# Performance work log

Measured on AMD Instinct MI355X. Metric: run time of the kernel, lower is better.

## Reference

```python
import jax, jax.numpy as jnp
import numpy as np

B, D = 512, 512
NOBJ, NWRD = 12, 16  # word_feat rows act as 'objects', object_feat rows as 'words' (arg swap in SentiGAT.forward)
N_OW = NOBJ + NWRD
EPS = 1e-12


def _with_self_loops(src, dst, n):
    return (np.concatenate([src, np.arange(n)]), np.concatenate([dst, np.arange(n)]))

_src = np.tile(np.arange(NOBJ), NWRD)                 # arange(n_obj).repeat(n_words) in torch == tile
_dst = np.repeat(np.arange(NWRD), NOBJ) + NOBJ        # repeat_interleave + offset
SRC_OW, DST_OW = map(jnp.asarray, _with_self_loops(_src, _dst, N_OW))

_E5 = np.array([[0,0,0,0,1,1,1,1,2,2,2,2,3,3,3,3,4,4,4,4],
                [1,2,3,4,0,2,3,4,0,1,3,4,0,1,2,4,0,1,2,3]])
SRC5, DST5 = map(jnp.asarray, _with_self_loops(_E5[0], _E5[1], 5))


def gat_conv(x, src, dst, W, a_src, a_dst, bias, concat, num_nodes):
    """PyG GATConv (add_self_loops already in src/dst, negative_slope=0.2, dropout=0)."""
    heads, out_dim = a_src.shape
    h = (x @ W).reshape(num_nodes, heads, out_dim)
    e = jax.nn.leaky_relu((h * a_src).sum(-1)[src] + (h * a_dst).sum(-1)[dst], 0.2)  # [E, heads]
    m = jax.ops.segment_max(e, dst, num_segments=num_nodes)
    p = jnp.exp(e - m[dst])
    alpha = p / jax.ops.segment_sum(p, dst, num_segments=num_nodes)[dst]             # softmax over incoming edges
    out = jax.ops.segment_sum(alpha[:, :, None] * h[src], dst, num_segments=num_nodes)
    out = out.reshape(num_nodes, heads * out_dim) if concat else out.mean(axis=1)
    return out + bias


def _ind_norm(f):
    # add_feature_indicator + F.normalize(p=2, dim=1, eps=1e-12)
    v = (f.sum(axis=1) != 0).astype(f.dtype)[:, None]
    g = jnp.concatenate([f, v], axis=1)
    return g / jnp.maximum(jnp.linalg.norm(g, axis=1, keepdims=True), EPS)


def setup_inputs() -> dict:
    k = jax.random.split(jax.random.key(0), 32)
    r = lambda i, s: jax.random.normal(k[i], s, dtype=jnp.float32)
    sc = 0.05
    return {
        "text_feat": r(0, (B, D)), "image_feat": r(1, (B, D)), "imgtxt_feat": r(2, (B, D)),
        "face_feat": r(3, (B, D)), "word_feat": r(4, (B, NOBJ, D)), "object_feat": r(5, (B, NWRD, D)),
        "ow_W": r(6, (D, 2 * D)) * sc, "ow_asrc": r(7, (2, D)) * sc, "ow_adst": r(8, (2, D)) * sc,
        "ow_b": jnp.zeros((D,), jnp.float32),
        "g1_W": r(9, (D + 1, D)) * sc, "g1_asrc": r(10, (1, D)) * sc, "g1_adst": r(11, (1, D)) * sc,
        "g1_b": jnp.zeros((D,), jnp.float32),
        "g2_W": r(12, (D, D)) * sc, "g2_asrc": r(13, (1, D)) * sc, "g2_adst": r(14, (1, D)) * sc,
        "g2_b": jnp.zeros((D,), jnp.float32),
        "m1_W": r(15, (5 * D, D)) * sc, "m1_b": jnp.zeros((D,), jnp.float32),
        "m2_W": r(16, (D, 3)) * sc, "m2_b": jnp.zeros((3,), jnp.float32),
    }


def reference(text_feat, image_feat, imgtxt_feat, face_feat, word_feat, object_feat,
              ow_W, ow_asrc, ow_adst, ow_b,
              g1_W, g1_asrc, g1_adst, g1_b,
              g2_W, g2_asrc, g2_adst, g2_b,
              m1_W, m1_b, m2_W, m2_b):
    # --- ObjectWordGAT (object_embs=word_feat, word_embs=object_feat per SentiGAT.forward) ---
    def per_sample(obj, wrd):
        x = jnp.concatenate([obj, wrd], axis=0)                       # [N_OW, D]
        h = gat_conv(x, SRC_OW, DST_OW, ow_W, ow_asrc, ow_adst, ow_b, False, N_OW)
        uo, uw = h[:NOBJ], h[NOBJ:]
        attn = jax.nn.softmax(uo @ uw.T, axis=1)                      # [NOBJ, NWRD]
        return (attn @ uw).mean(axis=0)                               # [D]
    aligned = jax.vmap(per_sample)(word_feat, object_feat)            # [B, D]

    feats = [_ind_norm(f) for f in (text_feat, image_feat, imgtxt_feat, face_feat, aligned)]
    x = jnp.stack(feats, axis=1)                                      # [B, 5, D+1]

    # edge_attr (cosine sims) is ignored by GATConv when edge_dim is None
    def graph5(xb):
        h = gat_conv(xb, SRC5, DST5, g1_W, g1_asrc, g1_adst, g1_b, True, 5)
        h = jax.nn.relu(h)
        return gat_conv(h, SRC5, DST5, g2_W, g2_asrc, g2_adst, g2_b, True, 5)
    x = jax.vmap(graph5)(x)                                           # [B, 5, D]

    fused = x.reshape(B, 5 * D)
    hid = jax.nn.relu(fused @ m1_W + m1_b)                            # dropout = identity (eval)
    return hid @ m2_W + m2_b                                          # [B, 3] logits
```

## Files before the change

kernel.cpp:

```cpp
#include <hip/hip_runtime.h>
#include <hip/hip_bf16.h>
#include <math.h>


#define B_SAMP 512

typedef short short8 __attribute__((ext_vector_type(8)));
typedef float floatx4 __attribute__((ext_vector_type(4)));

__device__ __forceinline__ float lrelu02(float x) { return x > 0.f ? x : 0.2f * x; }

__device__ __forceinline__ unsigned short cvt_bf16(float f) {
    union { float f; unsigned int u; } v; v.f = f;
    unsigned int u = v.u;
    return (unsigned short)((u + 0x7FFFu + ((u >> 16) & 1u)) >> 16);
}
__device__ __forceinline__ float bf2f(unsigned short u) {
    union { unsigned int u; float f; } v; v.u = ((unsigned int)u) << 16;
    return v.f;
}
__device__ __forceinline__ void gload_lds16(const unsigned short* g, unsigned short* l) {
    __builtin_amdgcn_global_load_lds(
        (const __attribute__((address_space(1))) void*)g,
        (__attribute__((address_space(3))) void*)l, 16, 0, 0);
}

__global__ __launch_bounds__(256) void prep(
    const float* __restrict__ ow_W, const float* __restrict__ ow_asrc,
    const float* __restrict__ ow_adst,
    const float* __restrict__ g1_W, const float* __restrict__ g2_W,
    const float* __restrict__ m1_W,
    float* __restrict__ vg, unsigned short* __restrict__ owWt,
    unsigned short* __restrict__ g1Wt, unsigned short* __restrict__ g2Wt,
    unsigned short* __restrict__ m1Wt)
{
    __shared__ float T[32][33];
    const int tid = threadIdx.x;
    int bid = blockIdx.x;

    if (bid < 128) {
        const int lane = tid & 63;
        const int gw = bid * 4 + (tid >> 6);
        for (int idx = gw; idx < 2048; idx += 512) {
            int t = idx >> 9, k = idx & 511;
            const float* a = (t < 2) ? (ow_asrc + t * 512) : (ow_adst + (t - 2) * 512);
            const float* wr = ow_W + (size_t)k * 1024 + (t & 1) * 512;
            float s = 0.f;
#pragma unroll
            for (int j = 0; j < 8; ++j) s += wr[lane + 64 * j] * a[lane + 64 * j];
            for (int off = 32; off > 0; off >>= 1) s += __shfl_down(s, off, 64);
            if (lane == 0) vg[idx] = s;
        }
        return;
    }
    bid -= 128;
    const float* W; int ldw, K, Kpad, koff, ktiles; float scale; unsigned short* Wt;
    if (bid < 256)        { W = ow_W;       ldw = 1024; K = 512;  Kpad = 1024; koff = 0;   scale = 0.5f; Wt = owWt; ktiles = 16; }
    else if (bid < 512)   { bid -= 256;  W = ow_W + 512; ldw = 1024; K = 512;  Kpad = 1024; koff = 512; scale = 0.5f; Wt = owWt; ktiles = 16; }
    else if (bid < 784)   { bid -= 512;  W = g1_W; ldw = 512; K = 513;  Kpad = 544;  koff = 0; scale = 1.f; Wt = g1Wt; ktiles = 17; }
    else if (bid < 1040)  { bid -= 784;  W = g2_W; ldw = 512; K = 512;  Kpad = 512;  koff = 0; scale = 1.f; Wt = g2Wt; ktiles = 16; }
    else                  { bid -= 1040; W = m1_W; ldw = 512; K = 2560; Kpad = 2560; koff = 0; scale = 1.f; Wt = m1Wt; ktiles = 80; }
    const int k0 = (bid % ktiles) * 32;
    const int n0 = (bid / ktiles) * 32;
    {
        int kr = tid >> 3, nc = (tid & 7) * 4;
        float4 v = make_float4(0.f, 0.f, 0.f, 0.f);
        if (k0 + kr < K) v = *(const float4*)(W + (size_t)(k0 + kr) * ldw + n0 + nc);
        T[nc + 0][kr] = v.x * scale; T[nc + 1][kr] = v.y * scale;
        T[nc + 2][kr] = v.z * scale; T[nc + 3][kr] = v.w * scale;
    }
    __syncthreads();
    {
        int nr = tid >> 3, kc = (tid & 7) * 4;
        ushort4 w;
        w.x = cvt_bf16(T[nr][kc + 0]);
        w.y = cvt_bf16(T[nr][kc + 1]);
        w.z = cvt_bf16(T[nr][kc + 2]);
        w.w = cvt_bf16(T[nr][kc + 3]);
        *(ushort4*)(Wt + (size_t)(n0 + nr) * Kpad + koff + k0 + kc) = w;
    }
}

__global__ __launch_bounds__(256) void ow_pre(
    const float* __restrict__ wf, const float* __restrict__ of,
    const float* __restrict__ vg,
    unsigned short* __restrict__ zcat)
{
    const int b = blockIdx.x;
    __shared__ float Xs[28][512];
    __shared__ float ss[28][2], sd[28][2];
    __shared__ float alpha[16][2][13];

    const int tid = threadIdx.x;
    const int lane = tid & 63;
    const int wid = tid >> 6;

    for (int idx = tid; idx < 28 * 128; idx += 256) {
        int n = idx >> 7, c = (idx & 127) * 4;
        const float* src = (n < 12) ? (wf + ((size_t)b * 12 + n) * 512)
                                    : (of + ((size_t)b * 16 + (n - 12)) * 512);
        *(float4*)&Xs[n][c] = *(const float4*)(src + c);
    }
    __syncthreads();

    for (int p = wid; p < 112; p += 4) {
        int n = p >> 2, t = p & 3;
        const float* vv = vg + t * 512;
        float s = 0.f;
#pragma unroll
        for (int j = 0; j < 8; ++j) s += Xs[n][lane + 64 * j] * vv[lane + 64 * j];
        for (int off = 32; off > 0; off >>= 1) s += __shfl_down(s, off, 64);
        if (lane == 0) { if (t < 2) ss[n][t] = s; else sd[n][t - 2] = s; }
    }
    __syncthreads();

    if (tid < 32) {
        int w = tid >> 1, h = tid & 1;
        float sdv = sd[12 + w][h];
        float e[13], mx = -1e30f;
        for (int j = 0; j < 12; ++j) { e[j] = lrelu02(ss[j][h] + sdv); mx = fmaxf(mx, e[j]); }
        e[12] = lrelu02(ss[12 + w][h] + sdv); mx = fmaxf(mx, e[12]);
        float den = 0.f;
        for (int j = 0; j < 13; ++j) { e[j] = expf(e[j] - mx); den += e[j]; }
        float inv = 1.f / den;
        for (int j = 0; j < 13; ++j) alpha[w][h][j] = e[j] * inv;
    }
    __syncthreads();

    unsigned short* zb = zcat + (size_t)b * 28 * 1024;
    for (int idx = tid; idx < 12 * 1024; idx += 256) {
        int n = idx >> 10, d = idx & 511;
        zb[idx] = cvt_bf16(Xs[n][d]);
    }
    for (int c = tid; c < 1024; c += 256) {
        int h = c >> 9, d = c & 511;
        float xr[12];
#pragma unroll
        for (int j = 0; j < 12; ++j) xr[j] = Xs[j][d];
#pragma unroll 4
        for (int w = 0; w < 16; ++w) {
            float a = alpha[w][h][12] * Xs[12 + w][d];
#pragma unroll
            for (int j = 0; j < 12; ++j) a += alpha[w][h][j] * xr[j];
            zb[(size_t)(12 + w) * 1024 + c] = cvt_bf16(a);
        }
    }
}

__global__ __launch_bounds__(256) void gemm_glds(
    const unsigned short* __restrict__ A, int lda,
    const unsigned short* __restrict__ Bt, int ldbt,
    unsigned short* __restrict__ C, int ldc,
    int K, const float* __restrict__ bias)
{
    __shared__ unsigned short As[2][64][32];
    __shared__ unsigned short Bs[2][128][32];

    const int tid = threadIdx.x;
    const int lane = tid & 63;
    const int wid = tid >> 6;

    const int bid = blockIdx.x;
    const int m = (bid >> 5) * 8 + (bid & 7);
    const int n = (bid >> 3) & 3;
    const int m0 = m * 64;
    const int n0 = n * 128;

    const int srow = lane >> 2;
    const int sseg = (lane & 3) * 8;
    const unsigned short* ga = A + (size_t)(m0 + wid * 16 + srow) * lda + sseg;
    const unsigned short* gb = Bt + (size_t)(n0 + wid * 32 + srow) * ldbt + sseg;
    const size_t b16 = (size_t)16 * ldbt;

#define STAGE(t, K0)                                              \
    do {                                                          \
        gload_lds16(ga + (K0), &As[t][wid * 16][0]);              \
        gload_lds16(gb + (K0), &Bs[t][wid * 32][0]);              \
        gload_lds16(gb + (K0) + b16, &Bs[t][wid * 32 + 16][0]);   \
    } while (0)

    const int wm = (wid & 1) * 32;
    const int wn = (wid >> 1) * 64;
    const int fr = lane & 15;
    const int kq = (lane >> 4) * 8;

    floatx4 acc[2][4];
#pragma unroll
    for (int i = 0; i < 2; ++i)
#pragma unroll
        for (int j = 0; j < 4; ++j) acc[i][j] = (floatx4){0.f, 0.f, 0.f, 0.f};

    STAGE(0, 0);
    __syncthreads();

    int t = 0;
    for (int k0 = 0; k0 < K; k0 += 32, t ^= 1) {
        if (k0 + 32 < K) STAGE(t ^ 1, k0 + 32);

        short8 af[2], bw[4];
#pragma unroll
        for (int i = 0; i < 2; ++i)
            af[i] = *(const short8*)&As[t][wm + i * 16 + fr][kq];
#pragma unroll
        for (int j = 0; j < 4; ++j)
            bw[j] = *(const short8*)&Bs[t][wn + j * 16 + fr][kq];
#pragma unroll
        for (int i = 0; i < 2; ++i)
#pragma unroll
            for (int j = 0; j < 4; ++j)
                acc[i][j] = __builtin_amdgcn_mfma_f32_16x16x32_bf16(
                    af[i], bw[j], acc[i][j], 0, 0, 0);
        __syncthreads();
    }
#undef STAGE

    const int fq = lane >> 4;
#pragma unroll
    for (int i = 0; i < 2; ++i) {
#pragma unroll
        for (int j = 0; j < 4; ++j) {
#pragma unroll
            for (int q = 0; q < 4; ++q) {
                int row = m0 + wm + i * 16 + fq * 4 + q;
                int col = n0 + wn + j * 16 + fr;
                C[(size_t)row * ldc + col] = cvt_bf16(acc[i][j][q] + bias[col]);
            }
        }
    }
}

template <int BM, int BN, int WGM, int RELU, int SPLITK, int OBF16>
__global__ __launch_bounds__(256) void gemm_v3(
    const unsigned short* __restrict__ A, int lda,
    const unsigned short* __restrict__ Bt, int ldbt,
    void* __restrict__ Cv, int ldc,
    int M, int N, int K,
    const float* __restrict__ bias)
{
    constexpr int WGN = 4 / WGM;
    constexpr int WM = BM / WGM, WN = BN / WGN;
    constexpr int MF = WM / 16, NF = WN / 16;
    constexpr int CA = (BM * 4 + 255) / 256, CB = (BN * 4 + 255) / 256;

    __shared__ unsigned short As[2][BM][40];
    __shared__ unsigned short Bs[2][BN][40];

    const int tid = threadIdx.x;
    const int m0 = blockIdx.x * BM;
    const int n0 = blockIdx.y * BN;
    const int lane = tid & 63;
    const int wid = tid >> 6;
    const int wm = (wid % WGM) * WM;
    const int wn = (wid / WGM) * WN;
    const int fr = lane & 15;
    const int kq = (lane >> 4) * 8;

    const int kchunk = K / SPLITK;
    const int kbeg = (SPLITK > 1) ? blockIdx.z * kchunk : 0;
    const int kend = kbeg + kchunk;
    float* Cf = (float*)Cv;
    unsigned short* Cb = (unsigned short*)Cv;
    if (SPLITK > 1) Cf += (size_t)blockIdx.z * M * ldc;

    short8 ra[CA], rb[CB];
#define LOADAB(K0)                                                                       \
    do {                                                                                 \
        _Pragma("unroll")                                                                \
        for (int c = 0; c < CA; ++c) {                                                   \
            int id = tid + c * 256;                                                      \
            if (BM * 4 % 256 == 0 || id < BM * 4)                                        \
                ra[c] = *(const short8*)(A + (size_t)(m0 + (id >> 2)) * lda + (K0) + (id & 3) * 8); \
        }                                                                                \
        _Pragma("unroll")                                                                \
        for (int c = 0; c < CB; ++c) {                                                   \
            int id = tid + c * 256;                                                      \
            if (BN * 4 % 256 == 0 || id < BN * 4)                                        \
                rb[c] = *(const short8*)(Bt + (size_t)(n0 + (id >> 2)) * ldbt + (K0) + (id & 3) * 8); \
        }                                                                                \
    } while (0)

    LOADAB(kbeg);

    floatx4 acc[MF][NF];
#pragma unroll
    for (int i = 0; i < MF; ++i)
#pragma unroll
        for (int j = 0; j < NF; ++j) acc[i][j] = (floatx4){0.f, 0.f, 0.f, 0.f};

    int t = 0;
    for (int k0 = kbeg; k0 < kend; k0 += 32, t ^= 1) {
#pragma unroll
        for (int c = 0; c < CA; ++c) {
            int id = tid + c * 256;
            if (BM * 4 % 256 == 0 || id < BM * 4)
                *(short8*)&As[t][id >> 2][(id & 3) * 8] = ra[c];
        }
#pragma unroll
        for (int c = 0; c < CB; ++c) {
            int id = tid + c * 256;
            if (BN * 4 % 256 == 0 || id < BN * 4)
                *(short8*)&Bs[t][id >> 2][(id & 3) * 8] = rb[c];
        }
        __syncthreads();
        if (k0 + 32 < kend) LOADAB(k0 + 32);

        short8 af[MF], bw[NF];
#pragma unroll
        for (int i = 0; i < MF; ++i)
            af[i] = *(const short8*)&As[t][wm + i * 16 + fr][kq];
#pragma unroll
        for (int j = 0; j < NF; ++j)
            bw[j] = *(const short8*)&Bs[t][wn + j * 16 + fr][kq];
#pragma unroll
        for (int i = 0; i < MF; ++i)
#pragma unroll
            for (int j = 0; j < NF; ++j)
                acc[i][j] = __builtin_amdgcn_mfma_f32_16x16x32_bf16(
                    af[i], bw[j], acc[i][j], 0, 0, 0);
    }
#undef LOADAB

    const int fq = lane >> 4;
#pragma unroll
    for (int i = 0; i < MF; ++i) {
#pragma unroll
        for (int j = 0; j < NF; ++j) {
#pragma unroll
            for (int q = 0; q < 4; ++q) {
                int row = m0 + wm + i * 16 + fq * 4 + q;
                int col = n0 + wn + j * 16 + fr;
                float v = acc[i][j][q];
                if (SPLITK == 1 && bias) v += bias[col];
                if (RELU) v = fmaxf(v, 0.f);
                if (OBF16) Cb[(size_t)row * ldc + col] = cvt_bf16(v);
                else       Cf[(size_t)row * ldc + col] = v;
            }
        }
    }
}

__global__ __launch_bounds__(256) void attn_x5(
    const unsigned short* __restrict__ hout,
    const float* __restrict__ tf, const float* __restrict__ im,
    const float* __restrict__ it, const float* __restrict__ fa,
    unsigned short* __restrict__ x5)
{
    const int b = blockIdx.x;
    __shared__ float uo[12][520];
    __shared__ float uw[16][520];
    __shared__ float S[12][16];
    __shared__ float w16[16];
    __shared__ float al[512];

    const int tid = threadIdx.x;
    const int lane = tid & 63;
    const int wid = tid >> 6;
    const unsigned short* hb = hout + (size_t)b * 28 * 512;

    for (int idx = tid; idx < 28 * 64; idx += 256) {
        int n = idx >> 6, c = (idx & 63) * 8;
        short8 v = *(const short8*)(hb + (size_t)n * 512 + c);
        float* row = (n < 12) ? &uo[n][c] : &uw[n - 12][c];
#pragma unroll
        for (int j = 0; j < 8; ++j) row[j] = bf2f((unsigned short)v[j]);
    }
    __syncthreads();

    for (int p = wid; p < 192; p += 4) {
        int i = p >> 4, j = p & 15;
        const float* ua = &uo[i][lane * 8];
        const float* uc = &uw[j][lane * 8];
        float s = 0.f;
#pragma unroll
        for (int d = 0; d < 8; ++d) s += ua[d] * uc[d];
        for (int off = 32; off > 0; off >>= 1) s += __shfl_down(s, off, 64);
        if (lane == 0) S[i][j] = s;
    }
    __syncthreads();

    if (tid < 12) {
        float mx = -1e30f;
        for (int j = 0; j < 16; ++j) mx = fmaxf(mx, S[tid][j]);
        float den = 0.f;
        for (int j = 0; j < 16; ++j) { float p = expf(S[tid][j] - mx); S[tid][j] = p; den += p; }
        float inv = 1.f / den;
        for (int j = 0; j < 16; ++j) S[tid][j] *= inv;
    }
    __syncthreads();

    if (tid < 16) {
        float s = 0.f;
        for (int i = 0; i < 12; ++i) s += S[i][tid];
        w16[tid] = s * (1.f / 12.f);
    }
    __syncthreads();

    for (int d = tid; d < 512; d += 256) {
        float s = 0.f;
#pragma unroll
        for (int j = 0; j < 16; ++j) s += w16[j] * uw[j][d];
        al[d] = s;
    }
    __syncthreads();

    for (int f = wid; f < 5; f += 4) {
        const float* src = (f == 0) ? tf : (f == 1) ? im : (f == 2) ? it : (f == 3) ? fa : nullptr;
        float vals[8];
        float sum = 0.f, sq = 0.f;
#pragma unroll
        for (int j = 0; j < 8; ++j) {
            float v = (f < 4) ? src[(size_t)b * 512 + lane + 64 * j] : al[lane + 64 * j];
            vals[j] = v;
            sum += v;
            sq += v * v;
        }
#pragma unroll
        for (int off = 32; off > 0; off >>= 1) {
            sum += __shfl_xor(sum, off, 64);
            sq  += __shfl_xor(sq,  off, 64);
        }
        float v = (sum != 0.f) ? 1.f : 0.f;
        float nrm = fmaxf(sqrtf(sq + v * v), 1e-12f);
        float inv = 1.f / nrm;
        unsigned short* dst = x5 + ((size_t)b * 5 + f) * 544;
#pragma unroll
        for (int j = 0; j < 8; ++j) dst[lane + 64 * j] = cvt_bf16(vals[j] * inv);
        if (lane == 0) dst[512] = cvt_bf16(v * inv);
        else if (lane < 32) dst[512 + lane] = 0;
    }
}

template <int RELU>
__global__ __launch_bounds__(256) void g5_gat(
    const unsigned short* __restrict__ Hg,
    const float* __restrict__ asrc, const float* __restrict__ adst,
    const float* __restrict__ bias, unsigned short* __restrict__ outp)
{
    const int b = blockIdx.x;
    __shared__ float ss[5], sd[5];
    __shared__ float alpha[5][5];

    const int tid = threadIdx.x;
    const int lane = tid & 63;
    const int wave = tid >> 6;
    const unsigned short* Hb = Hg + (size_t)b * 5 * 512;

    for (int p = wave; p < 10; p += 4) {
        int n = p >> 1, ty = p & 1;
        const unsigned short* hv = Hb + n * 512;
        const float* av = ty ? adst : asrc;
        float s = 0.f;
#pragma unroll
        for (int j = 0; j < 8; ++j) s += bf2f(hv[lane + 64 * j]) * av[lane + 64 * j];
        for (int off = 32; off > 0; off >>= 1) s += __shfl_down(s, off, 64);
        if (lane == 0) { if (ty) sd[n] = s; else ss[n] = s; }
    }
    __syncthreads();

    if (tid < 5) {
        int dn = tid;
        float e[5];
        float mx = -1e30f;
        for (int s = 0; s < 5; ++s) {
            e[s] = lrelu02(ss[s] + sd[dn]);
            mx = fmaxf(mx, e[s]);
        }
        float den = 0.f;
        for (int s = 0; s < 5; ++s) { e[s] = expf(e[s] - mx); den += e[s]; }
        float inv = 1.f / den;
        for (int s = 0; s < 5; ++s) alpha[dn][s] = e[s] * inv;
    }
    __syncthreads();

    for (int d = tid; d < 512; d += 256) {
        float h0 = bf2f(Hb[0 * 512 + d]), h1 = bf2f(Hb[1 * 512 + d]), h2 = bf2f(Hb[2 * 512 + d]);
        float h3 = bf2f(Hb[3 * 512 + d]), h4 = bf2f(Hb[4 * 512 + d]);
        float bd = bias[d];
#pragma unroll
        for (int dn = 0; dn < 5; ++dn) {
            float v = alpha[dn][0] * h0 + alpha[dn][1] * h1 + alpha[dn][2] * h2 +
                      alpha[dn][3] * h3 + alpha[dn][4] * h4 + bd;
            if (RELU) v = fmaxf(v, 0.f);
            outp[((size_t)b * 5 + dn) * 512 + d] = cvt_bf16(v);
        }
    }
}

__global__ __launch_bounds__(64) void final2(
    const float* __restrict__ parts, const float* __restrict__ b1,
    const float* __restrict__ w, const float* __restrict__ bvec,
    float* __restrict__ out)
{
    const int b = blockIdx.x;
    const int lane = threadIdx.x;
    float a0 = 0.f, a1 = 0.f, a2 = 0.f;
#pragma unroll
    for (int j = 0; j < 8; ++j) {
        int d = lane + 64 * j;
        size_t o = (size_t)b * 512 + d;
        float x = parts[o] + parts[262144 + o] + parts[524288 + o] + parts[786432 + o] + b1[d];
        x = fmaxf(x, 0.f);
        a0 += x * w[d * 3 + 0];
        a1 += x * w[d * 3 + 1];
        a2 += x * w[d * 3 + 2];
    }
    for (int off = 32; off > 0; off >>= 1) {
        a0 += __shfl_down(a0, off, 64);
        a1 += __shfl_down(a1, off, 64);
        a2 += __shfl_down(a2, off, 64);
    }
    if (lane == 0) {
        out[b * 3 + 0] = a0 + bvec[0];
        out[b * 3 + 1] = a1 + bvec[1];
        out[b * 3 + 2] = a2 + bvec[2];
    }
}

extern "C" void kernel_launch(void* const* d_in, const int* in_sizes, int n_in,
                              void* d_out, int out_size, void* d_ws, size_t ws_size,
                              hipStream_t stream) {
    const float* text   = (const float*)d_in[0];
    const float* image  = (const float*)d_in[1];
    const float* imgtxt = (const float*)d_in[2];
    const float* face   = (const float*)d_in[3];
    const float* word   = (const float*)d_in[4];
    const float* obj    = (const float*)d_in[5];
    const float* ow_W    = (const float*)d_in[6];
    const float* ow_asrc = (const float*)d_in[7];
    const float* ow_adst = (const float*)d_in[8];
    const float* ow_b    = (const float*)d_in[9];
    const float* g1_W    = (const float*)d_in[10];
    const float* g1_asrc = (const float*)d_in[11];
    const float* g1_adst = (const float*)d_in[12];
    const float* g1_b    = (const float*)d_in[13];
    const float* g2_W    = (const float*)d_in[14];
    const float* g2_asrc = (const float*)d_in[15];
    const float* g2_adst = (const float*)d_in[16];
    const float* g2_b    = (const float*)d_in[17];
    const float* m1_W    = (const float*)d_in[18];
    const float* m1_b    = (const float*)d_in[19];
    const float* m2_W    = (const float*)d_in[20];
    const float* m2_b    = (const float*)d_in[21];

    float* ws = (float*)d_ws;
    float* vg = ws;
    float* hidp = ws + 2048;
    unsigned short* owWt = (unsigned short*)(hidp + 1048576);
    unsigned short* g1Wt = owWt + 524288;
    unsigned short* g2Wt = g1Wt + 278528;
    unsigned short* m1Wt = g2Wt + 262144;
    unsigned short* zcat = m1Wt + 1310720;
    unsigned short* houtb = zcat + 14680064;
    unsigned short* x5b  = houtb + 7340032;
    unsigned short* h1b  = x5b + 1392640;
    unsigned short* fsb  = h1b + 1310720;
    unsigned short* hgb  = fsb + 1310720;

    prep<<<2448, 256, 0, stream>>>(ow_W, ow_asrc, ow_adst, g1_W, g2_W, m1_W,
                                   vg, owWt, g1Wt, g2Wt, m1Wt);

    ow_pre<<<B_SAMP, 256, 0, stream>>>(word, obj, vg, zcat);
    gemm_glds<<<896, 256, 0, stream>>>(
        zcat, 1024, owWt, 1024, houtb, 512, 1024, ow_b);
    attn_x5<<<B_SAMP, 256, 0, stream>>>(houtb, text, image, imgtxt, face, x5b);

    gemm_v3<64, 64, 2, 0, 1, 1><<<dim3(40, 8), 256, 0, stream>>>(
        x5b, 544, g1Wt, 544, hgb, 512, 2560, 512, 544, nullptr);
    g5_gat<1><<<B_SAMP, 256, 0, stream>>>(hgb, g1_asrc, g1_adst, g1_b, h1b);
    gemm_v3<64, 64, 2, 0, 1, 1><<<dim3(40, 8), 256, 0, stream>>>(
        h1b, 512, g2Wt, 512, hgb, 512, 2560, 512, 512, nullptr);
    g5_gat<0><<<B_SAMP, 256, 0, stream>>>(hgb, g2_asrc, g2_adst, g2_b, fsb);

    gemm_v3<64, 64, 2, 0, 4, 0><<<dim3(8, 8, 4), 256, 0, stream>>>(
        fsb, 2560, m1Wt, 2560, hidp, 512, 512, 512, 2560, nullptr);
    final2<<<B_SAMP, 64, 0, stream>>>(hidp, m1_b, m2_W, m2_b, (float*)d_out);
}
```

Before: 128.6 us.

## Exploit self-loop-only object nodes: halve K via pre-summed head weights

Object nodes in the word-object GAT only receive their self-loop, so their head-mean output equals x·(W_h0+W_h1)/2. Prep now builds a pre-summed bf16 weight (WsR) and a second GEMM branch multiplies the raw fp32 word features by it with K=512, instead of carrying them through the concatenated K=1024 path. The zcat buffer shrinks to word rows only, and attn_x5 reads the two separate outputs. This cuts GEMM FLOPs and memory traffic for 12 of the 28 nodes per sample, but the new branch uses register-staged loads with inline fp32-to-bf16 conversion rather than direct global-to-LDS loads.

```diff
diff --git a/kernel.cpp b/kernel.cpp
--- a/kernel.cpp
+++ b/kernel.cpp
@@ -32,15 +32,16 @@
     const float* __restrict__ m1_W,
     float* __restrict__ vg, unsigned short* __restrict__ owWt,
     unsigned short* __restrict__ g1Wt, unsigned short* __restrict__ g2Wt,
-    unsigned short* __restrict__ m1Wt)
+    unsigned short* __restrict__ m1Wt, unsigned short* __restrict__ WsR)
 {
     __shared__ float T[32][33];
     const int tid = threadIdx.x;
     int bid = blockIdx.x;
+    const int lane = tid & 63;
+    const int wid = tid >> 6;
 
     if (bid < 128) {
-        const int lane = tid & 63;
-        const int gw = bid * 4 + (tid >> 6);
+        const int gw = bid * 4 + wid;
         for (int idx = gw; idx < 2048; idx += 512) {
             int t = idx >> 9, k = idx & 511;
             const float* a = (t < 2) ? (ow_asrc + t * 512) : (ow_adst + (t - 2) * 512);
@@ -55,17 +56,25 @@
     }
     bid -= 128;
     const float* W; int ldw, K, Kpad, koff, ktiles; float scale; unsigned short* Wt;
+    int sumh = 0;
     if (bid < 256)        { W = ow_W;       ldw = 1024; K = 512;  Kpad = 1024; koff = 0;   scale = 0.5f; Wt = owWt; ktiles = 16; }
     else if (bid < 512)   { bid -= 256;  W = ow_W + 512; ldw = 1024; K = 512;  Kpad = 1024; koff = 512; scale = 0.5f; Wt = owWt; ktiles = 16; }
     else if (bid < 784)   { bid -= 512;  W = g1_W; ldw = 512; K = 513;  Kpad = 544;  koff = 0; scale = 1.f; Wt = g1Wt; ktiles = 17; }
     else if (bid < 1040)  { bid -= 784;  W = g2_W; ldw = 512; K = 512;  Kpad = 512;  koff = 0; scale = 1.f; Wt = g2Wt; ktiles = 16; }
-    else                  { bid -= 1040; W = m1_W; ldw = 512; K = 2560; Kpad = 2560; koff = 0; scale = 1.f; Wt = m1Wt; ktiles = 80; }
+    else if (bid < 2320)  { bid -= 1040; W = m1_W; ldw = 512; K = 2560; Kpad = 2560; koff = 0; scale = 1.f; Wt = m1Wt; ktiles = 80; }
+    else                  { bid -= 2320; W = ow_W; ldw = 1024; K = 512; Kpad = 512; koff = 0; scale = 0.5f; Wt = WsR; ktiles = 16; sumh = 1; }
     const int k0 = (bid % ktiles) * 32;
     const int n0 = (bid / ktiles) * 32;
     {
         int kr = tid >> 3, nc = (tid & 7) * 4;
         float4 v = make_float4(0.f, 0.f, 0.f, 0.f);
-        if (k0 + kr < K) v = *(const float4*)(W + (size_t)(k0 + kr) * ldw + n0 + nc);
+        if (k0 + kr < K) {
+            v = *(const float4*)(W + (size_t)(k0 + kr) * ldw + n0 + nc);
+            if (sumh) {
+                float4 v2 = *(const float4*)(W + (size_t)(k0 + kr) * ldw + 512 + n0 + nc);
+                v.x += v2.x; v.y += v2.y; v.z += v2.z; v.w += v2.w;
+            }
+        }
         T[nc + 0][kr] = v.x * scale; T[nc + 1][kr] = v.y * scale;
         T[nc + 2][kr] = v.z * scale; T[nc + 3][kr] = v.w * scale;
     }
@@ -81,10 +90,10 @@
     }
 }
 
-__global__ __launch_bounds__(256) void ow_pre(
+__global__ __launch_bounds__(256) void ow_zw(
     const float* __restrict__ wf, const float* __restrict__ of,
     const float* __restrict__ vg,
-    unsigned short* __restrict__ zcat)
+    unsigned short* __restrict__ zw)
 {
     const int b = blockIdx.x;
     __shared__ float Xs[28][512];
@@ -127,31 +136,37 @@
     }
     __syncthreads();
 
-    unsigned short* zb = zcat + (size_t)b * 28 * 1024;
-    for (int idx = tid; idx < 12 * 1024; idx += 256) {
-        int n = idx >> 10, d = idx & 511;
-        zb[idx] = cvt_bf16(Xs[n][d]);
-    }
-    for (int c = tid; c < 1024; c += 256) {
-        int h = c >> 9, d = c & 511;
-        float xr[12];
-#pragma unroll
-        for (int j = 0; j < 12; ++j) xr[j] = Xs[j][d];
+    const int c4 = tid * 4;
+    const int h = tid >> 7;
+    const int d = c4 & 511;
+    float4 xr[12];
+#pragma unroll
+    for (int j = 0; j < 12; ++j) xr[j] = *(const float4*)&Xs[j][d];
+    unsigned short* zb = zw + (size_t)b * 16 * 1024;
 #pragma unroll 4
-        for (int w = 0; w < 16; ++w) {
-            float a = alpha[w][h][12] * Xs[12 + w][d];
-#pragma unroll
-            for (int j = 0; j < 12; ++j) a += alpha[w][h][j] * xr[j];
-            zb[(size_t)(12 + w) * 1024 + c] = cvt_bf16(a);
-        }
-    }
-}
-
-__global__ __launch_bounds__(256) void gemm_glds(
-    const unsigned short* __restrict__ A, int lda,
-    const unsigned short* __restrict__ Bt, int ldbt,
-    unsigned short* __restrict__ C, int ldc,
-    int K, const float* __restrict__ bias)
+    for (int w = 0; w < 16; ++w) {
+        const float* al = &alpha[w][h][0];
+        float4 xw = *(const float4*)&Xs[12 + w][d];
+        float a0 = al[12] * xw.x, a1 = al[12] * xw.y, a2 = al[12] * xw.z, a3 = al[12] * xw.w;
+#pragma unroll
+        for (int j = 0; j < 12; ++j) {
+            a0 += al[j] * xr[j].x; a1 += al[j] * xr[j].y;
+            a2 += al[j] * xr[j].z; a3 += al[j] * xr[j].w;
+        }
+        ushort4 o;
+        o.x = cvt_bf16(a0); o.y = cvt_bf16(a1); o.z = cvt_bf16(a2); o.w = cvt_bf16(a3);
+        *(ushort4*)(zb + (size_t)w * 1024 + c4) = o;
+    }
+}
+
+__global__ __launch_bounds__(256) void gemm_a1(
+    const unsigned short* __restrict__ zw,
+    const unsigned short* __restrict__ owWt,
+    const float* __restrict__ word,
+    const unsigned short* __restrict__ WsR,
+    const float* __restrict__ bias,
+    unsigned short* __restrict__ houtW,
+    unsigned short* __restrict__ houtO)
 {
     __shared__ unsigned short As[2][64][32];
     __shared__ unsigned short Bs[2][128][32];
@@ -159,73 +174,217 @@
     const int tid = threadIdx.x;
     const int lane = tid & 63;
     const int wid = tid >> 6;
-
     const int bid = blockIdx.x;
-    const int m = (bid >> 5) * 8 + (bid & 7);
-    const int n = (bid >> 3) & 3;
-    const int m0 = m * 64;
-    const int n0 = n * 128;
-
-    const int srow = lane >> 2;
-    const int sseg = (lane & 3) * 8;
-    const unsigned short* ga = A + (size_t)(m0 + wid * 16 + srow) * lda + sseg;
-    const unsigned short* gb = Bt + (size_t)(n0 + wid * 32 + srow) * ldbt + sseg;
-    const size_t b16 = (size_t)16 * ldbt;
-
-#define STAGE(t, K0)                                              \
+
+    const int wm = (wid & 1) * 32;
+    const int wn = (wid >> 1) * 64;
+    const int fr = lane & 15;
+    const int kq = (lane >> 4) * 8;
+    const int fq = lane >> 4;
+
+    floatx4 acc[2][4];
+#pragma unroll
+    for (int i = 0; i < 2; ++i)
+#pragma unroll
+        for (int j = 0; j < 4; ++j) acc[i][j] = (floatx4){0.f, 0.f, 0.f, 0.f};
+
+    if (bid < 512) {
+        const int m0 = (bid & 127) * 64;
+        const int n0 = (bid >> 7) * 128;
+        const int srow = lane >> 2;
+        const int sseg = (lane & 3) * 8;
+        const unsigned short* ga = zw + (size_t)(m0 + wid * 16 + srow) * 1024 + sseg;
+        const unsigned short* gb = owWt + (size_t)(n0 + wid * 32 + srow) * 1024 + sseg;
+        const size_t b16 = (size_t)16 * 1024;
+
+#define STAGEW(t, K0)                                             \
     do {                                                          \
         gload_lds16(ga + (K0), &As[t][wid * 16][0]);              \
         gload_lds16(gb + (K0), &Bs[t][wid * 32][0]);              \
         gload_lds16(gb + (K0) + b16, &Bs[t][wid * 32 + 16][0]);   \
     } while (0)
 
-    const int wm = (wid & 1) * 32;
-    const int wn = (wid >> 1) * 64;
-    const int fr = lane & 15;
-    const int kq = (lane >> 4) * 8;
-
-    floatx4 acc[2][4];
-#pragma unroll
-    for (int i = 0; i < 2; ++i)
-#pragma unroll
-        for (int j = 0; j < 4; ++j) acc[i][j] = (floatx4){0.f, 0.f, 0.f, 0.f};
-
-    STAGE(0, 0);
-    __syncthreads();
-
-    int t = 0;
-    for (int k0 = 0; k0 < K; k0 += 32, t ^= 1) {
-        if (k0 + 32 < K) STAGE(t ^ 1, k0 + 32);
-
-        short8 af[2], bw[4];
+        STAGEW(0, 0);
+        __syncthreads();
+        int t = 0;
+        for (int k0 = 0; k0 < 1024; k0 += 32, t ^= 1) {
+            if (k0 + 32 < 1024) STAGEW(t ^ 1, k0 + 32);
+            short8 af[2], bw[4];
+#pragma unroll
+            for (int i = 0; i < 2; ++i)
+                af[i] = *(const short8*)&As[t][wm + i * 16 + fr][kq];
+#pragma unroll
+            for (int j = 0; j < 4; ++j)
+                bw[j] = *(const short8*)&Bs[t][wn + j * 16 + fr][kq];
+#pragma unroll
+            for (int i = 0; i < 2; ++i)
+#pragma unroll
+                for (int j = 0; j < 4; ++j)
+                    acc[i][j] = __builtin_amdgcn_mfma_f32_16x16x32_bf16(
+                        af[i], bw[j], acc[i][j], 0, 0, 0);
+            __syncthreads();
+        }
+#undef STAGEW
 #pragma unroll
         for (int i = 0; i < 2; ++i)
-            af[i] = *(const short8*)&As[t][wm + i * 16 + fr][kq];
-#pragma unroll
-        for (int j = 0; j < 4; ++j)
-            bw[j] = *(const short8*)&Bs[t][wn + j * 16 + fr][kq];
+#pragma unroll
+            for (int j = 0; j < 4; ++j)
+#pragma unroll
+                for (int q = 0; q < 4; ++q) {
+                    int row = m0 + wm + i * 16 + fq * 4 + q;
+                    int col = n0 + wn + j * 16 + fr;
+                    houtW[(size_t)row * 512 + col] = cvt_bf16(acc[i][j][q] + bias[col]);
+                }
+    } else {
+        const int tb = bid - 512;
+        const int m0 = (tb % 96) * 64;
+        const int n0 = (tb / 96) * 128;
+
+        float4 raf[2]; short8 rb[2];
+#define LOADO(K0)                                                                  \
+    do {                                                                           \
+        _Pragma("unroll")                                                          \
+        for (int c = 0; c < 2; ++c) {                                              \
+            int id = tid + c * 256;                                                \
+            raf[c] = *(const float4*)(word + (size_t)(m0 + (id >> 3)) * 512 + (K0) + (id & 7) * 4); \
+            rb[c]  = *(const short8*)(WsR + (size_t)(n0 + (id >> 2)) * 512 + (K0) + (id & 3) * 8);  \
+        }                                                                          \
+    } while (0)
+
+        LOADO(0);
+        int t = 0;
+        for (int k0 = 0; k0 < 512; k0 += 32, t ^= 1) {
+#pragma unroll
+            for (int c = 0; c < 2; ++c) {
+                int id = tid + c * 256;
+                ushort4 w;
+                w.x = cvt_bf16(raf[c].x); w.y = cvt_bf16(raf[c].y);
+                w.z = cvt_bf16(raf[c].z); w.w = cvt_bf16(raf[c].w);
+                *(ushort4*)&As[t][id >> 3][(id & 7) * 4] = w;
+                *(short8*)&Bs[t][id >> 2][(id & 3) * 8] = rb[c];
+            }
+            __syncthreads();
+            if (k0 + 32 < 512) LOADO(k0 + 32);
+            short8 af[2], bw[4];
+#pragma unroll
+            for (int i = 0; i < 2; ++i)
+                af[i] = *(const short8*)&As[t][wm + i * 16 + fr][kq];
+#pragma unroll
+            for (int j = 0; j < 4; ++j)
+                bw[j] = *(const short8*)&Bs[t][wn + j * 16 + fr][kq];
+#pragma unroll
+            for (int i = 0; i < 2; ++i)
+#pragma unroll
+                for (int j = 0; j < 4; ++j)
+                    acc[i][j] = __builtin_amdgcn_mfma_f32_16x16x32_bf16(
+                        af[i], bw[j], acc[i][j], 0, 0, 0);
+        }
+#undef LOADO
 #pragma unroll
         for (int i = 0; i < 2; ++i)
 #pragma unroll
             for (int j = 0; j < 4; ++j)
-                acc[i][j] = __builtin_amdgcn_mfma_f32_16x16x32_bf16(
-                    af[i], bw[j], acc[i][j], 0, 0, 0);
-        __syncthreads();
-    }
-#undef STAGE
-
-    const int fq = lane >> 4;
-#pragma unroll
-    for (int i = 0; i < 2; ++i) {
-#pragma unroll
-        for (int j = 0; j < 4; ++j) {
-#pragma unroll
-            for (int q = 0; q < 4; ++q) {
-                int row = m0 + wm + i * 16 + fq * 4 + q;
-                int col = n0 + wn + j * 16 + fr;
-                C[(size_t)row * ldc + col] = cvt_bf16(acc[i][j][q] + bias[col]);
-            }
-        }
+#pragma unroll
+                for (int q = 0; q < 4; ++q) {
+                    int row = m0 + wm + i * 16 + fq * 4 + q;
+                    int col = n0 + wn + j * 16 + fr;
+                    houtO[(size_t)row * 512 + col] = cvt_bf16(acc[i][j][q] + bias[col]);
+                }
+    }
+}
+
+__global__ __launch_bounds__(256) void attn_x5(
+    const unsigned short* __restrict__ houtO,
+    const unsigned short* __restrict__ houtW,
+    const float* __restrict__ tf, const float* __restrict__ im,
+    const float* __restrict__ it, const float* __restrict__ fa,
+    unsigned short* __restrict__ x5)
+{
+    const int b = blockIdx.x;
+    __shared__ float uo[12][520];
+    __shared__ float uw[16][520];
+    __shared__ float S[12][16];
+    __shared__ float w16[16];
+    __shared__ float al[512];
+
+    const int tid = threadIdx.x;
+    const int lane = tid & 63;
+    const int wid = tid >> 6;
+    const unsigned short* ho = houtO + (size_t)b * 12 * 512;
+    const unsigned short* hw = houtW + (size_t)b * 16 * 512;
+
+    for (int idx = tid; idx < 28 * 64; idx += 256) {
+        int n = idx >> 6, c = (idx & 63) * 8;
+        const unsigned short* src = (n < 12) ? (ho + (size_t)n * 512 + c)
+                                             : (hw + (size_t)(n - 12) * 512 + c);
+        short8 v = *(const short8*)src;
+        float* row = (n < 12) ? &uo[n][c] : &uw[n - 12][c];
+#pragma unroll
+        for (int j = 0; j < 8; ++j) row[j] = bf2f((unsigned short)v[j]);
+    }
+    __syncthreads();
+
+    for (int p = wid; p < 192; p += 4) {
+        int i = p >> 4, j = p & 15;
+        const float* ua = &uo[i][lane * 8];
+        const float* uc = &uw[j][lane * 8];
+        float s = 0.f;
+#pragma unroll
+        for (int d = 0; d < 8; ++d) s += ua[d] * uc[d];
+        for (int off = 32; off > 0; off >>= 1) s += __shfl_down(s, off, 64);
+        if (lane == 0) S[i][j] = s;
+    }
+    __syncthreads();
+
+    if (tid < 12) {
+        float mx = -1e30f;
+        for (int j = 0; j < 16; ++j) mx = fmaxf(mx, S[tid][j]);
+        float den = 0.f;
+        for (int j = 0; j < 16; ++j) { float p = expf(S[tid][j] - mx); S[tid][j] = p; den += p; }
+        float inv = 1.f / den;
+        for (int j = 0; j < 16; ++j) S[tid][j] *= inv;
+    }
+    __syncthreads();
+
+    if (tid < 16) {
+        float s = 0.f;
+        for (int i = 0; i < 12; ++i) s += S[i][tid];
+        w16[tid] = s * (1.f / 12.f);
+    }
+    __syncthreads();
+
+    for (int d = tid; d < 512; d += 256) {
+        float s = 0.f;
+#pragma unroll
+        for (int j = 0; j < 16; ++j) s += w16[j] * uw[j][d];
+        al[d] = s;
+    }
+    __syncthreads();
+
+    for (int f = wid; f < 5; f += 4) {
+        const float* src = (f == 0) ? tf : (f == 1) ? im : (f == 2) ? it : (f == 3) ? fa : nullptr;
+        float vals[8];
+        float sum = 0.f, sq = 0.f;
+#pragma unroll
+        for (int j = 0; j < 8; ++j) {
+            float v = (f < 4) ? src[(size_t)b * 512 + lane + 64 * j] : al[lane + 64 * j];
+            vals[j] = v;
+            sum += v;
+            sq += v * v;
+        }
+#pragma unroll
+        for (int off = 32; off > 0; off >>= 1) {
+            sum += __shfl_xor(sum, off, 64);
+            sq  += __shfl_xor(sq,  off, 64);
+        }
+        float v = (sum != 0.f) ? 1.f : 0.f;
+        float nrm = fmaxf(sqrtf(sq + v * v), 1e-12f);
+        float inv = 1.f / nrm;
+        unsigned short* dst = x5 + ((size_t)b * 5 + f) * 544;
+#pragma unroll
+        for (int j = 0; j < 8; ++j) dst[lane + 64 * j] = cvt_bf16(vals[j] * inv);
+        if (lane == 0) dst[512] = cvt_bf16(v * inv);
+        else if (lane < 32) dst[512 + lane] = 0;
     }
 }
 
@@ -336,97 +495,6 @@
                 else       Cf[(size_t)row * ldc + col] = v;
             }
         }
-    }
-}
-
-__global__ __launch_bounds__(256) void attn_x5(
-    const unsigned short* __restrict__ hout,
-    const float* __restrict__ tf, const float* __restrict__ im,
-    const float* __restrict__ it, const float* __restrict__ fa,
-    unsigned short* __restrict__ x5)
-{
-    const int b = blockIdx.x;
-    __shared__ float uo[12][520];
-    __shared__ float uw[16][520];
-    __shared__ float S[12][16];
-    __shared__ float w16[16];
-    __shared__ float al[512];
-
-    const int tid = threadIdx.x;
-    const int lane = tid & 63;
-    const int wid = tid >> 6;
-    const unsigned short* hb = hout + (size_t)b * 28 * 512;
-
-    for (int idx = tid; idx < 28 * 64; idx += 256) {
-        int n = idx >> 6, c = (idx & 63) * 8;
-        short8 v = *(const short8*)(hb + (size_t)n * 512 + c);
-        float* row = (n < 12) ? &uo[n][c] : &uw[n - 12][c];
-#pragma unroll
-        for (int j = 0; j < 8; ++j) row[j] = bf2f((unsigned short)v[j]);
-    }
-    __syncthreads();
-
-    for (int p = wid; p < 192; p += 4) {
-        int i = p >> 4, j = p & 15;
-        const float* ua = &uo[i][lane * 8];
-        const float* uc = &uw[j][lane * 8];
-        float s = 0.f;
-#pragma unroll
-        for (int d = 0; d < 8; ++d) s += ua[d] * uc[d];
-        for (int off = 32; off > 0; off >>= 1) s += __shfl_down(s, off, 64);
-        if (lane == 0) S[i][j] = s;
-    }
-    __syncthreads();
-
-    if (tid < 12) {
-        float mx = -1e30f;
-        for (int j = 0; j < 16; ++j) mx = fmaxf(mx, S[tid][j]);
-        float den = 0.f;
-        for (int j = 0; j < 16; ++j) { float p = expf(S[tid][j] - mx); S[tid][j] = p; den += p; }
-        float inv = 1.f / den;
-        for (int j = 0; j < 16; ++j) S[tid][j] *= inv;
-    }
-    __syncthreads();
-
-    if (tid < 16) {
-        float s = 0.f;
-        for (int i = 0; i < 12; ++i) s += S[i][tid];
-        w16[tid] = s * (1.f / 12.f);
-    }
-    __syncthreads();
-
-    for (int d = tid; d < 512; d += 256) {
-        float s = 0.f;
-#pragma unroll
-        for (int j = 0; j < 16; ++j) s += w16[j] * uw[j][d];
-        al[d] = s;
-    }
-    __syncthreads();
-
-    for (int f = wid; f < 5; f += 4) {
-        const float* src = (f == 0) ? tf : (f == 1) ? im : (f == 2) ? it : (f == 3) ? fa : nullptr;
-        float vals[8];
-        float sum = 0.f, sq = 0.f;
-#pragma unroll
-        for (int j = 0; j < 8; ++j) {
-            float v = (f < 4) ? src[(size_t)b * 512 + lane + 64 * j] : al[lane + 64 * j];
-            vals[j] = v;
-            sum += v;
-            sq += v * v;
-        }
-#pragma unroll
-        for (int off = 32; off > 0; off >>= 1) {
-            sum += __shfl_xor(sum, off, 64);
-            sq  += __shfl_xor(sq,  off, 64);
-        }
-        float v = (sum != 0.f) ? 1.f : 0.f;
-        float nrm = fmaxf(sqrtf(sq + v * v), 1e-12f);
-        float inv = 1.f / nrm;
-        unsigned short* dst = x5 + ((size_t)b * 5 + f) * 544;
-#pragma unroll
-        for (int j = 0; j < 8; ++j) dst[lane + 64 * j] = cvt_bf16(vals[j] * inv);
-        if (lane == 0) dst[512] = cvt_bf16(v * inv);
-        else if (lane < 32) dst[512 + lane] = 0;
     }
 }
 
@@ -543,26 +611,27 @@
     const float* m2_b    = (const float*)d_in[21];
 
     float* ws = (float*)d_ws;
-    float* vg = ws;
+    float* vg   = ws;
     float* hidp = ws + 2048;
-    unsigned short* owWt = (unsigned short*)(hidp + 1048576);
-    unsigned short* g1Wt = owWt + 524288;
-    unsigned short* g2Wt = g1Wt + 278528;
-    unsigned short* m1Wt = g2Wt + 262144;
-    unsigned short* zcat = m1Wt + 1310720;
-    unsigned short* houtb = zcat + 14680064;
-    unsigned short* x5b  = houtb + 7340032;
-    unsigned short* h1b  = x5b + 1392640;
-    unsigned short* fsb  = h1b + 1310720;
-    unsigned short* hgb  = fsb + 1310720;
-
-    prep<<<2448, 256, 0, stream>>>(ow_W, ow_asrc, ow_adst, g1_W, g2_W, m1_W,
-                                   vg, owWt, g1Wt, g2Wt, m1Wt);
-
-    ow_pre<<<B_SAMP, 256, 0, stream>>>(word, obj, vg, zcat);
-    gemm_glds<<<896, 256, 0, stream>>>(
-        zcat, 1024, owWt, 1024, houtb, 512, 1024, ow_b);
-    attn_x5<<<B_SAMP, 256, 0, stream>>>(houtb, text, image, imgtxt, face, x5b);
+    unsigned short* owWt  = (unsigned short*)(hidp + 1048576);
+    unsigned short* WsR   = owWt + 524288;
+    unsigned short* g1Wt  = WsR + 262144;
+    unsigned short* g2Wt  = g1Wt + 278528;
+    unsigned short* m1Wt  = g2Wt + 262144;
+    unsigned short* zw    = m1Wt + 1310720;
+    unsigned short* houtW = zw + 8388608;
+    unsigned short* houtO = houtW + 4194304;
+    unsigned short* x5b   = houtO + 3145728;
+    unsigned short* h1b   = x5b + 1392640;
+    unsigned short* fsb   = h1b + 1310720;
+    unsigned short* hgb   = fsb + 1310720;
+
+    prep<<<2704, 256, 0, stream>>>(ow_W, ow_asrc, ow_adst, g1_W, g2_W, m1_W,
+                                   vg, owWt, g1Wt, g2Wt, m1Wt, WsR);
+
+    ow_zw<<<B_SAMP, 256, 0, stream>>>(word, obj, vg, zw);
+    gemm_a1<<<896, 256, 0, stream>>>(zw, owWt, word, WsR, ow_b, houtW, houtO);
+    attn_x5<<<B_SAMP, 256, 0, stream>>>(houtO, houtW, text, image, imgtxt, face, x5b);
 
     gemm_v3<64, 64, 2, 0, 1, 1><<<dim3(40, 8), 256, 0, stream>>>(
         x5b, 544, g1Wt, 544, hgb, 512, 2560, 512, 544, nullptr);
```

After: 131.5 us. 2.3% more time.
